# Kernel optimization log

Measured on AMD Instinct MI355X. Metric: run time of the kernel, lower is better.

The kernel has to match this reference:

```python
import jax, jax.numpy as jnp
import numpy as np
from jax import lax

N, L, D, F = 16, 512, 256, 256
KW = 3
EPS = 1e-5


def setup_inputs() -> dict:
    key = jax.random.key(0)
    ks = jax.random.split(key, 12)
    return {
        "x": jax.random.normal(ks[0], (N, L, D), jnp.float32),
        "conv1_w": jax.random.normal(ks[1], (F, D, KW), jnp.float32) * 0.05,
        "conv1_b": jnp.zeros((F,), jnp.float32),
        "ln1_g": jnp.ones((F,), jnp.float32),
        "ln1_b": jnp.zeros((F,), jnp.float32),
        "conv2_w": jax.random.normal(ks[2], (F, F, KW), jnp.float32) * 0.05,
        "conv2_b": jnp.zeros((F,), jnp.float32),
        "ln2_g": jnp.ones((F,), jnp.float32),
        "ln2_b": jnp.zeros((F,), jnp.float32),
        "lin_w": jax.random.normal(ks[3], (F, 1), jnp.float32) * 0.05,
        "lin_b": jnp.zeros((1,), jnp.float32),
        "target": jax.random.randint(ks[4], (N, L), 1, 8, jnp.int32),
        "mel_max_length": 4096,
    }


def _layernorm(h, g, b):
    m = jnp.mean(h, axis=-1, keepdims=True)
    v = jnp.var(h, axis=-1, keepdims=True)
    return (h - m) * lax.rsqrt(v + EPS) * g + b


def _conv1d(h, w, b):
    # h: [N, L, C_in]; w: [C_out, C_in, K]; 'same' padding=1 for K=3
    y = lax.conv_general_dilated(h.transpose(0, 2, 1), w, (1,), [(1, 1)],
                                 dimension_numbers=("NCH", "OIH", "NCH"))
    return (y + b[None, :, None]).transpose(0, 2, 1)


def _duration_predictor(x, c1w, c1b, g1, b1, c2w, c2b, g2, b2, lw, lb):
    h = jax.nn.relu(_layernorm(_conv1d(x, c1w, c1b), g1, b1))
    h = jax.nn.relu(_layernorm(_conv1d(h, c2w, c2b), g2, b2))
    return jax.nn.relu(h @ lw + lb)[..., 0]  # [N, L]


def _length_regulate(x, dur, T):
    # Equivalent to one-hot alignment @ x, done as a duration-indexed gather.
    cum = jnp.cumsum(dur, axis=-1)                       # [N, L]
    t = jnp.arange(T, dtype=cum.dtype)                   # [T]
    idx = jax.vmap(lambda c: jnp.searchsorted(c, t, side="right"))(cum)  # [N, T]
    valid = t[None, :] < cum[:, -1:]                     # [N, T]
    out = jnp.take_along_axis(x, jnp.clip(idx, 0, x.shape[1] - 1)[:, :, None], axis=1)
    return jnp.where(valid[..., None], out, jnp.zeros((), x.dtype))


def reference(x, conv1_w, conv1_b, ln1_g, ln1_b, conv2_w, conv2_b, ln2_g, ln2_b,
              lin_w, lin_b, target, mel_max_length):
    dpo = _duration_predictor(x, conv1_w, conv1_b, ln1_g, ln1_b,
                              conv2_w, conv2_b, ln2_g, ln2_b, lin_w, lin_b)
    out = _length_regulate(x, target, mel_max_length)    # [N, mel_max_length, D]
    return (out, dpo)
```

## Files before the change

### kernel.cpp

```cpp
#include <hip/hip_runtime.h>
#include <hip/hip_bf16.h>

using u16 = unsigned short;
typedef __bf16 bf16x8 __attribute__((ext_vector_type(8)));
typedef float f32x4 __attribute__((ext_vector_type(4)));

#define N_B   16
#define L_S   512
#define D_F   256
#define T_MEL 4096
#define M_TOT (N_B * L_S)
#define OUT_ELEMS ((size_t)N_B * T_MEL * D_F)
#define H1_ELEMS  ((size_t)M_TOT * D_F)
#define WP_ELEMS  (24 * 8192)
#define TBLK 128

__device__ __forceinline__ u16 f2bf(float f) {
  __hip_bfloat16 h = __float2bfloat16(f);
  return *(u16*)&h;
}

__device__ __forceinline__ bf16x8 pack8(float4 v0, float4 v1) {
  union { bf16x8 h; u16 u[8]; } r;
  r.u[0] = f2bf(v0.x); r.u[1] = f2bf(v0.y); r.u[2] = f2bf(v0.z); r.u[3] = f2bf(v0.w);
  r.u[4] = f2bf(v1.x); r.u[5] = f2bf(v1.y); r.u[6] = f2bf(v1.z); r.u[7] = f2bf(v1.w);
  return r.h;
}

__global__ __launch_bounds__(256)
void pack_kernel(const float* __restrict__ w1, const float* __restrict__ w2,
                 u16* __restrict__ wp1, u16* __restrict__ wp2) {
  int o   = (int)blockIdx.x * 256 + (int)threadIdx.x;
  int s   = o >> 13;
  int rem = o & 8191;
  int f   = rem >> 5;
  int ki  = rem & 31;
  int d   = ((s & 7) << 5) + ki;
  int tap = s >> 3;
  int src = f * 768 + d * 3 + tap;
  wp1[o] = f2bf(w1[src]);
  wp2[o] = f2bf(w2[src]);
}

template<int STAGE>
__device__ __forceinline__ void conv_body(
    const int blk, const int t,
    const float* __restrict__ Xf, const u16* __restrict__ Xh,
    const u16* __restrict__ Wp,
    const float* __restrict__ cb,  const float* __restrict__ lgm,
    const float* __restrict__ lbt, const float* __restrict__ lw,
    const float* __restrict__ lb,  u16* __restrict__ Hout,
    float* __restrict__ dpo,
    u16* As, u16* Bs, float* sBias, float* sG, float* sB, float* sLw,
    float (*redS)[4][16], float (*redQ)[4][16])
{
  if (t < 256) {
    sBias[t] = cb[t];
    sG[t]    = lgm[t];
    sB[t]    = lbt[t];
    if (STAGE == 2) sLw[t] = lw[t];
  }

  const int m0   = blk * 32;
  const int n    = m0 >> 9;
  const int l0   = m0 & 511;
  const int wave = t >> 6, lane = t & 63;
  const int cs   = wave & 3;
  const int rh   = wave >> 2;
  const int wc   = cs * 64;
  const int rh16 = rh * 16;
  const int p    = lane & 15, q = lane >> 4;

  f32x4 acc[4];
  #pragma unroll
  for (int i = 0; i < 4; i++) acc[i] = (f32x4){0.f, 0.f, 0.f, 0.f};

  auto LDW = [&](int s, uint4 &r0, uint4 &r1) {
    const u16* src = Wp + ((size_t)s << 13);
    r0 = *(const uint4*)(src + (t << 3));
    r1 = *(const uint4*)(src + ((t + 512) << 3));
  };
  auto WRB = [&](int buf, const uint4 &r0, const uint4 &r1) {
    *(uint4*)(Bs + (buf << 13) + (t << 3))         = r0;
    *(uint4*)(Bs + (buf << 13) + ((t + 512) << 3)) = r1;
  };
  auto MF = [&](int buf, int s) {
    const u16* bs = Bs + (buf << 13);
    const int tap = s >> 3, dbase = (s & 7) << 5;
    bf16x8 af = *(const bf16x8*)(As + (rh16 + p + tap) * 264 + dbase + (q << 3));
    #pragma unroll
    for (int ct = 0; ct < 4; ct++) {
      bf16x8 bfr = *(const bf16x8*)(bs + ((wc + ct * 16 + p) << 5) + (q << 3));
      acc[ct] = __builtin_amdgcn_mfma_f32_16x16x32_bf16(af, bfr, acc[ct], 0, 0, 0);
    }
  };

  uint4 e0, e1, o0, o1;
  LDW(0, e0, e1);
  LDW(1, o0, o1);

  for (int c = t; c < 1088; c += 512) {
    int row  = c >> 5;
    int col8 = c & 31;
    int l    = l0 + row - 1;
    uint4 val;
    if ((unsigned)l < 512u) {
      if (STAGE == 1) {
        const float* src = Xf + (((size_t)((n << 9) + l)) << 8) + (col8 << 3);
        float4 v0 = *(const float4*)src;
        float4 v1 = *(const float4*)(src + 4);
        bf16x8 pk = pack8(v0, v1);
        __builtin_memcpy(&val, &pk, 16);
      } else {
        val = *(const uint4*)(Xh + (((size_t)((n << 9) + l)) << 8) + (col8 << 3));
      }
    } else {
      val = make_uint4(0u, 0u, 0u, 0u);
    }
    *(uint4*)(As + row * 264 + (col8 << 3)) = val;
  }
  WRB(0, e0, e1);
  __syncthreads();

  for (int s2 = 0; s2 < 24; s2 += 2) {
    MF(0, s2);
    if (s2 + 2 < 24) LDW(s2 + 2, e0, e1);
    WRB(1, o0, o1);
    __syncthreads();
    MF(1, s2 + 1);
    if (s2 + 3 < 24) LDW(s2 + 3, o0, o1);
    if (s2 + 2 < 24) WRB(0, e0, e1);
    __syncthreads();
  }

  float s0[4] = {0,0,0,0}, s1[4] = {0,0,0,0};
  #pragma unroll
  for (int ct = 0; ct < 4; ct++) {
    float bias = sBias[wc + ct * 16 + p];
    #pragma unroll
    for (int j = 0; j < 4; j++) {
      float v = acc[ct][j] + bias;
      acc[ct][j] = v;
      s0[j] += v;
      s1[j] += v * v;
    }
  }
  #pragma unroll
  for (int m = 1; m <= 8; m <<= 1) {
    #pragma unroll
    for (int j = 0; j < 4; j++) {
      s0[j] += __shfl_xor(s0[j], m);
      s1[j] += __shfl_xor(s1[j], m);
    }
  }
  if (p == 0) {
    #pragma unroll
    for (int j = 0; j < 4; j++) {
      redS[rh][cs][q * 4 + j] = s0[j];
      redQ[rh][cs][q * 4 + j] = s1[j];
    }
  }
  __syncthreads();
  float mean[4], rstd[4];
  #pragma unroll
  for (int j = 0; j < 4; j++) {
    int r = q * 4 + j;
    float S = redS[rh][0][r] + redS[rh][1][r] + redS[rh][2][r] + redS[rh][3][r];
    float Q = redQ[rh][0][r] + redQ[rh][1][r] + redQ[rh][2][r] + redQ[rh][3][r];
    float mu  = S * (1.0f / 256.0f);
    float var = Q * (1.0f / 256.0f) - mu * mu;
    mean[j] = mu;
    rstd[j] = rsqrtf(var + 1e-5f);
  }

  if (STAGE == 1) {
    #pragma unroll
    for (int ct = 0; ct < 4; ct++) {
      int c = wc + ct * 16 + p;
      float gg = sG[c], bb = sB[c];
      #pragma unroll
      for (int j = 0; j < 4; j++) {
        float v = (acc[ct][j] - mean[j]) * rstd[j] * gg + bb;
        v = fmaxf(v, 0.0f);
        Hout[(size_t)(m0 + rh16 + q * 4 + j) * 256 + c] = f2bf(v);
      }
    }
  } else {
    float ls[4] = {0,0,0,0};
    #pragma unroll
    for (int ct = 0; ct < 4; ct++) {
      int c = wc + ct * 16 + p;
      float gg = sG[c], bb = sB[c], ww = sLw[c];
      #pragma unroll
      for (int j = 0; j < 4; j++) {
        float v = (acc[ct][j] - mean[j]) * rstd[j] * gg + bb;
        v = fmaxf(v, 0.0f);
        ls[j] += v * ww;
      }
    }
    #pragma unroll
    for (int m = 1; m <= 8; m <<= 1) {
      #pragma unroll
      for (int j = 0; j < 4; j++) ls[j] += __shfl_xor(ls[j], m);
    }
    __syncthreads();
    if (p == 0) {
      #pragma unroll
      for (int j = 0; j < 4; j++) redS[rh][cs][q * 4 + j] = ls[j];
    }
    __syncthreads();
    if (t < 32) {
      int r2 = t >> 4, ri = t & 15;
      float dv = fmaxf(redS[r2][0][ri] + redS[r2][1][ri] +
                       redS[r2][2][ri] + redS[r2][3][ri] + lb[0], 0.0f);
      dpo[m0 + t] = dv;
    }
  }
}

__device__ __forceinline__ void lr_body512(
    const int lrblk, const int t,
    const float* __restrict__ X, const int* __restrict__ tgt,
    float* __restrict__ out, int* sc, int* sidx)
{
  const int n  = lrblk >> 4;
  const int t0 = (lrblk & 15) * 256;

  sc[t] = tgt[n * L_S + t];
  __syncthreads();
  for (int off = 1; off < L_S; off <<= 1) {
    int v = (t >= off) ? sc[t - off] : 0;
    __syncthreads();
    sc[t] += v;
    __syncthreads();
  }
  const int total = sc[L_S - 1];
  if (t < 256) {
    int tt = t0 + t;
    int lo = 0, hi = L_S;
    while (lo < hi) {
      int mid = (lo + hi) >> 1;
      if (sc[mid] <= tt) lo = mid + 1; else hi = mid;
    }
    sidx[t] = (tt < total) ? lo : -1;
  }
  __syncthreads();

  #pragma unroll
  for (int i = 0; i < 32; i++) {
    int u   = t + i * 512;
    int dg  = u & 63;
    int tr  = u >> 6;
    int idx = sidx[tr];
    float4 v = make_float4(0.f, 0.f, 0.f, 0.f);
    if (idx >= 0)
      v = *(const float4*)(X + (((size_t)(n * L_S + idx)) << 8) + dg * 4);
    *(float4*)(out + (((size_t)(n * T_MEL + t0 + tr)) << 8) + dg * 4) = v;
  }
}

template<int STAGE>
__global__ __launch_bounds__(512)
void conv_ln_kernel(const float* __restrict__ Xf, const u16* __restrict__ Xh,
                    const u16* __restrict__ Wp,
                    const float* __restrict__ cb,  const float* __restrict__ lgm,
                    const float* __restrict__ lbt, const float* __restrict__ lw,
                    const float* __restrict__ lb,  u16* __restrict__ Hout,
                    float* __restrict__ dpo)
{
  __shared__ __align__(16) u16 As[34 * 264 + 8];
  __shared__ __align__(16) u16 Bs[2 * 8192];
  __shared__ float sBias[256], sG[256], sB[256], sLw[256];
  __shared__ float redS[2][4][16], redQ[2][4][16];
  conv_body<STAGE>((int)blockIdx.x, (int)threadIdx.x, Xf, Xh, Wp, cb, lgm, lbt,
                   lw, lb, Hout, dpo, As, Bs, sBias, sG, sB, sLw, redS, redQ);
}

__global__ __launch_bounds__(512)
void conv1_lr_kernel(const float* __restrict__ x, const u16* __restrict__ Wp,
                     const float* __restrict__ cb,  const float* __restrict__ lgm,
                     const float* __restrict__ lbt, u16* __restrict__ Hout,
                     const int* __restrict__ tgt, float* __restrict__ out)
{
  __shared__ __align__(16) u16 As[34 * 264 + 8];
  __shared__ __align__(16) u16 Bs[2 * 8192];
  __shared__ float sBias[256], sG[256], sB[256], sLw[256];
  __shared__ float redS[2][4][16], redQ[2][4][16];
  __shared__ int  sc[512];
  __shared__ int  sidx[256];

  const int blk = (int)blockIdx.x, t = (int)threadIdx.x;
  if (blk < 256) {
    conv_body<1>(blk, t, x, nullptr, Wp, cb, lgm, lbt, nullptr, nullptr,
                 Hout, nullptr, As, Bs, sBias, sG, sB, sLw, redS, redQ);
  } else {
    lr_body512(blk - 256, t, x, tgt, out, sc, sidx);
  }
}

__global__ __launch_bounds__(256)
void lr_kernel(const float* __restrict__ X, const int* __restrict__ tgt,
               float* __restrict__ out) {
  __shared__ int c[L_S];
  __shared__ int sidx[TBLK];
  const int t  = threadIdx.x;
  const int n  = blockIdx.x >> 5;
  const int t0 = (blockIdx.x & 31) * TBLK;

  c[t]       = tgt[n * L_S + t];
  c[t + 256] = tgt[n * L_S + t + 256];
  __syncthreads();
  for (int off = 1; off < L_S; off <<= 1) {
    int v0 = (t >= off) ? c[t - off] : 0;
    int i1 = t + 256;
    int v1 = (i1 >= off) ? c[i1 - off] : 0;
    __syncthreads();
    c[t]  += v0;
    c[i1] += v1;
    __syncthreads();
  }
  const int total = c[L_S - 1];
  if (t < TBLK) {
    int tt = t0 + t;
    int lo = 0, hi = L_S;
    while (lo < hi) {
      int mid = (lo + hi) >> 1;
      if (c[mid] <= tt) lo = mid + 1; else hi = mid;
    }
    sidx[t] = (tt < total) ? lo : -1;
  }
  __syncthreads();

  #pragma unroll
  for (int i = 0; i < 32; i++) {
    int u   = t + i * 256;
    int dg  = u & 63;
    int tr  = u >> 6;
    int idx = sidx[tr];
    float4 v = make_float4(0.f, 0.f, 0.f, 0.f);
    if (idx >= 0)
      v = *(const float4*)(X + (((size_t)(n * L_S + idx)) << 8) + dg * 4);
    *(float4*)(out + (((size_t)(n * T_MEL + t0 + tr)) << 8) + dg * 4) = v;
  }
}

extern "C" void kernel_launch(void* const* d_in, const int* in_sizes, int n_in,
                              void* d_out, int out_size, void* d_ws, size_t ws_size,
                              hipStream_t stream) {
  (void)in_sizes; (void)n_in; (void)out_size;

  const float* x   = (const float*)d_in[0];
  const float* w1  = (const float*)d_in[1];
  const float* b1  = (const float*)d_in[2];
  const float* g1  = (const float*)d_in[3];
  const float* be1 = (const float*)d_in[4];
  const float* w2  = (const float*)d_in[5];
  const float* b2  = (const float*)d_in[6];
  const float* g2  = (const float*)d_in[7];
  const float* be2 = (const float*)d_in[8];
  const float* lw  = (const float*)d_in[9];
  const float* lb  = (const float*)d_in[10];
  const int*   tgt = (const int*)d_in[11];

  float* out = (float*)d_out;
  float* dpo = out + OUT_ELEMS;

  const size_t need = (H1_ELEMS + 2 * (size_t)WP_ELEMS) * sizeof(u16);

  if (d_ws != nullptr && ws_size >= need) {
    u16* h1  = (u16*)d_ws;
    u16* wp1 = h1 + H1_ELEMS;
    u16* wp2 = wp1 + WP_ELEMS;
    pack_kernel<<<768, 256, 0, stream>>>(w1, w2, wp1, wp2);
    conv1_lr_kernel<<<512, 512, 0, stream>>>(x, wp1, b1, g1, be1, h1, tgt, out);
    conv_ln_kernel<2><<<M_TOT / 32, 512, 0, stream>>>(
        nullptr, h1, wp2, b2, g2, be2, lw, lb, nullptr, dpo);
  } else {
    u16* h1  = (u16*)d_out;
    u16* wp1 = h1 + H1_ELEMS;
    u16* wp2 = wp1 + WP_ELEMS;
    pack_kernel<<<768, 256, 0, stream>>>(w1, w2, wp1, wp2);
    conv_ln_kernel<1><<<M_TOT / 32, 512, 0, stream>>>(
        x, nullptr, wp1, b1, g1, be1, nullptr, nullptr, h1, nullptr);
    conv_ln_kernel<2><<<M_TOT / 32, 512, 0, stream>>>(
        nullptr, h1, wp2, b2, g2, be2, lw, lb, nullptr, dpo);
    lr_kernel<<<N_B * (T_MEL / TBLK), 256, 0, stream>>>(x, tgt, out);
  }
}
```

Baseline: 121.0 us.

## Fuse both conv+layernorm stages and length regulation into one kernel

Merges the conv1 and conv2 stages into a single kernel: each block recomputes conv1 over a 66-row halo window (32 output rows plus a one-row halo on each side, rounded up for MFMA tiles) and keeps the intermediate H tile in shared memory. This removes the global round-trip of the bf16 intermediate and one kernel launch. In exchange it does about twice the conv1 MFMA work per block and uses more shared memory, which may lower occupancy. The length-regulation blocks still share the same launch.

```diff
diff --git a/kernel.cpp b/kernel.cpp
--- a/kernel.cpp
+++ b/kernel.cpp
@@ -40,6 +40,325 @@
   int src = f * 768 + d * 3 + tap;
   wp1[o] = f2bf(w1[src]);
   wp2[o] = f2bf(w2[src]);
+}
+
+__device__ __forceinline__ void lr_body512(
+    const int lrblk, const int t,
+    const float* __restrict__ X, const int* __restrict__ tgt,
+    float* __restrict__ out, int* sc, int* sidx)
+{
+  const int n  = lrblk >> 4;
+  const int t0 = (lrblk & 15) * 256;
+
+  sc[t] = tgt[n * L_S + t];
+  __syncthreads();
+  for (int off = 1; off < L_S; off <<= 1) {
+    int v = (t >= off) ? sc[t - off] : 0;
+    __syncthreads();
+    sc[t] += v;
+    __syncthreads();
+  }
+  const int total = sc[L_S - 1];
+  if (t < 256) {
+    int tt = t0 + t;
+    int lo = 0, hi = L_S;
+    while (lo < hi) {
+      int mid = (lo + hi) >> 1;
+      if (sc[mid] <= tt) lo = mid + 1; else hi = mid;
+    }
+    sidx[t] = (tt < total) ? lo : -1;
+  }
+  __syncthreads();
+
+  #pragma unroll
+  for (int i = 0; i < 32; i++) {
+    int u   = t + i * 512;
+    int dg  = u & 63;
+    int tr  = u >> 6;
+    int idx = sidx[tr];
+    float4 v = make_float4(0.f, 0.f, 0.f, 0.f);
+    if (idx >= 0)
+      v = *(const float4*)(X + (((size_t)(n * L_S + idx)) << 8) + dg * 4);
+    *(float4*)(out + (((size_t)(n * T_MEL + t0 + tr)) << 8) + dg * 4) = v;
+  }
+}
+
+__global__ __launch_bounds__(512)
+void fused_conv_lr_kernel(
+    const float* __restrict__ x,
+    const u16* __restrict__ wp1, const u16* __restrict__ wp2,
+    const float* __restrict__ b1, const float* __restrict__ g1,
+    const float* __restrict__ e1p,
+    const float* __restrict__ b2, const float* __restrict__ g2,
+    const float* __restrict__ e2p,
+    const float* __restrict__ lw, const float* __restrict__ lb,
+    const int* __restrict__ tgt, float* __restrict__ out,
+    float* __restrict__ dpo)
+{
+  __shared__ __align__(16) u16 As66[66 * 264];
+  __shared__ __align__(16) u16 Hs[34 * 264];
+  __shared__ __align__(16) u16 Bs[2 * 8192];
+  __shared__ float sB1[256], sG1[256], sE1[256];
+  __shared__ float sB2[256], sG2[256], sE2[256], sLw[256];
+  __shared__ float redS[4][4][16], redQ[4][4][16];
+  __shared__ int  sc[512];
+  __shared__ int  sidx[256];
+
+  const int blk = (int)blockIdx.x, t = (int)threadIdx.x;
+  if (blk >= 256) {
+    lr_body512(blk - 256, t, x, tgt, out, sc, sidx);
+    return;
+  }
+
+  if (t < 256) {
+    sB1[t] = b1[t];  sG1[t] = g1[t];  sE1[t] = e1p[t];
+    sB2[t] = b2[t];  sG2[t] = g2[t];  sE2[t] = e2p[t];
+    sLw[t] = lw[t];
+  }
+
+  const int m0   = blk * 32;
+  const int n    = m0 >> 9;
+  const int l0   = m0 & 511;
+  const int wave = t >> 6, lane = t & 63;
+  const int cs   = wave & 3;
+  const int rha  = wave >> 2;
+  const int wc   = cs * 64;
+  const int p    = lane & 15, q = lane >> 4;
+
+  auto LDW = [&](const u16* Wp, int s, uint4 &r0, uint4 &r1) {
+    const u16* src = Wp + ((size_t)s << 13);
+    r0 = *(const uint4*)(src + (t << 3));
+    r1 = *(const uint4*)(src + ((t + 512) << 3));
+  };
+  auto WRB = [&](int buf, const uint4 &r0, const uint4 &r1) {
+    *(uint4*)(Bs + (buf << 13) + (t << 3))         = r0;
+    *(uint4*)(Bs + (buf << 13) + ((t + 512) << 3)) = r1;
+  };
+
+  f32x4 acc1[2][4];
+  #pragma unroll
+  for (int gi = 0; gi < 2; gi++)
+    #pragma unroll
+    for (int i = 0; i < 4; i++) acc1[gi][i] = (f32x4){0.f, 0.f, 0.f, 0.f};
+
+  auto MF1 = [&](int buf, int s) {
+    const u16* bs = Bs + (buf << 13);
+    const int tap = s >> 3, dbase = (s & 7) << 5;
+    bf16x8 af0 = *(const bf16x8*)(As66 + ((rha << 4)        + p + tap) * 264 + dbase + (q << 3));
+    bf16x8 af1 = *(const bf16x8*)(As66 + (((rha + 2) << 4)  + p + tap) * 264 + dbase + (q << 3));
+    #pragma unroll
+    for (int ct = 0; ct < 4; ct++) {
+      bf16x8 bfr = *(const bf16x8*)(bs + ((wc + ct * 16 + p) << 5) + (q << 3));
+      acc1[0][ct] = __builtin_amdgcn_mfma_f32_16x16x32_bf16(af0, bfr, acc1[0][ct], 0, 0, 0);
+      acc1[1][ct] = __builtin_amdgcn_mfma_f32_16x16x32_bf16(af1, bfr, acc1[1][ct], 0, 0, 0);
+    }
+  };
+
+  uint4 e0, e1, o0, o1;
+  LDW(wp1, 0, e0, e1);
+  LDW(wp1, 1, o0, o1);
+
+  for (int c = t; c < 66 * 32; c += 512) {
+    int row  = c >> 5;
+    int col8 = c & 31;
+    int l    = l0 - 17 + row;
+    uint4 val = make_uint4(0u, 0u, 0u, 0u);
+    if ((unsigned)l < 512u) {
+      const float* src = x + (((size_t)((n << 9) + l)) << 8) + (col8 << 3);
+      float4 v0 = *(const float4*)src;
+      float4 v1 = *(const float4*)(src + 4);
+      bf16x8 pk = pack8(v0, v1);
+      __builtin_memcpy(&val, &pk, 16);
+    }
+    *(uint4*)(As66 + row * 264 + (col8 << 3)) = val;
+  }
+  WRB(0, e0, e1);
+  __syncthreads();
+
+  for (int s2 = 0; s2 < 24; s2 += 2) {
+    MF1(0, s2);
+    if (s2 + 2 < 24) LDW(wp1, s2 + 2, e0, e1);
+    WRB(1, o0, o1);
+    __syncthreads();
+    MF1(1, s2 + 1);
+    if (s2 + 3 < 24) LDW(wp1, s2 + 3, o0, o1);
+    if (s2 + 2 < 24) WRB(0, e0, e1);
+    __syncthreads();
+  }
+
+  {
+    float s0[2][4] = {{0,0,0,0},{0,0,0,0}}, s1[2][4] = {{0,0,0,0},{0,0,0,0}};
+    #pragma unroll
+    for (int gi = 0; gi < 2; gi++)
+      #pragma unroll
+      for (int ct = 0; ct < 4; ct++) {
+        float bias = sB1[wc + ct * 16 + p];
+        #pragma unroll
+        for (int j = 0; j < 4; j++) {
+          float v = acc1[gi][ct][j] + bias;
+          acc1[gi][ct][j] = v;
+          s0[gi][j] += v;
+          s1[gi][j] += v * v;
+        }
+      }
+    #pragma unroll
+    for (int m = 1; m <= 8; m <<= 1)
+      #pragma unroll
+      for (int gi = 0; gi < 2; gi++)
+        #pragma unroll
+        for (int j = 0; j < 4; j++) {
+          s0[gi][j] += __shfl_xor(s0[gi][j], m);
+          s1[gi][j] += __shfl_xor(s1[gi][j], m);
+        }
+    if (p == 0) {
+      #pragma unroll
+      for (int gi = 0; gi < 2; gi++) {
+        int g = rha + gi * 2;
+        #pragma unroll
+        for (int j = 0; j < 4; j++) {
+          redS[g][cs][q * 4 + j] = s0[gi][j];
+          redQ[g][cs][q * 4 + j] = s1[gi][j];
+        }
+      }
+    }
+    __syncthreads();
+    float mean[2][4], rstd[2][4];
+    #pragma unroll
+    for (int gi = 0; gi < 2; gi++) {
+      int g = rha + gi * 2;
+      #pragma unroll
+      for (int j = 0; j < 4; j++) {
+        int r = q * 4 + j;
+        float S = redS[g][0][r] + redS[g][1][r] + redS[g][2][r] + redS[g][3][r];
+        float Q = redQ[g][0][r] + redQ[g][1][r] + redQ[g][2][r] + redQ[g][3][r];
+        float mu  = S * (1.0f / 256.0f);
+        float var = Q * (1.0f / 256.0f) - mu * mu;
+        mean[gi][j] = mu;
+        rstd[gi][j] = rsqrtf(var + 1e-5f);
+      }
+    }
+    #pragma unroll
+    for (int gi = 0; gi < 2; gi++) {
+      int g = rha + gi * 2;
+      #pragma unroll
+      for (int ct = 0; ct < 4; ct++) {
+        int c = wc + ct * 16 + p;
+        float gg = sG1[c], bb = sE1[c];
+        #pragma unroll
+        for (int j = 0; j < 4; j++) {
+          float v = (acc1[gi][ct][j] - mean[gi][j]) * rstd[gi][j] * gg + bb;
+          v = fmaxf(v, 0.0f);
+          int hidx = (g << 4) - 15 + q * 4 + j;
+          if ((unsigned)hidx < 34u)
+            Hs[hidx * 264 + c] = f2bf(v);
+        }
+      }
+    }
+    __syncthreads();
+    if (l0 == 0   && t < 132) ((unsigned*)Hs)[t] = 0u;
+    if (l0 == 480 && t < 132) ((unsigned*)Hs)[33 * 132 + t] = 0u;
+    __syncthreads();
+  }
+
+  f32x4 acc2[4];
+  #pragma unroll
+  for (int i = 0; i < 4; i++) acc2[i] = (f32x4){0.f, 0.f, 0.f, 0.f};
+
+  auto MF2 = [&](int buf, int s) {
+    const u16* bs = Bs + (buf << 13);
+    const int tap = s >> 3, dbase = (s & 7) << 5;
+    bf16x8 af = *(const bf16x8*)(Hs + ((rha << 4) + p + tap) * 264 + dbase + (q << 3));
+    #pragma unroll
+    for (int ct = 0; ct < 4; ct++) {
+      bf16x8 bfr = *(const bf16x8*)(bs + ((wc + ct * 16 + p) << 5) + (q << 3));
+      acc2[ct] = __builtin_amdgcn_mfma_f32_16x16x32_bf16(af, bfr, acc2[ct], 0, 0, 0);
+    }
+  };
+
+  LDW(wp2, 0, e0, e1);
+  LDW(wp2, 1, o0, o1);
+  WRB(0, e0, e1);
+  __syncthreads();
+
+  for (int s2 = 0; s2 < 24; s2 += 2) {
+    MF2(0, s2);
+    if (s2 + 2 < 24) LDW(wp2, s2 + 2, e0, e1);
+    WRB(1, o0, o1);
+    __syncthreads();
+    MF2(1, s2 + 1);
+    if (s2 + 3 < 24) LDW(wp2, s2 + 3, o0, o1);
+    if (s2 + 2 < 24) WRB(0, e0, e1);
+    __syncthreads();
+  }
+
+  {
+    float s0[4] = {0,0,0,0}, s1[4] = {0,0,0,0};
+    #pragma unroll
+    for (int ct = 0; ct < 4; ct++) {
+      float bias = sB2[wc + ct * 16 + p];
+      #pragma unroll
+      for (int j = 0; j < 4; j++) {
+        float v = acc2[ct][j] + bias;
+        acc2[ct][j] = v;
+        s0[j] += v;
+        s1[j] += v * v;
+      }
+    }
+    #pragma unroll
+    for (int m = 1; m <= 8; m <<= 1)
+      #pragma unroll
+      for (int j = 0; j < 4; j++) {
+        s0[j] += __shfl_xor(s0[j], m);
+        s1[j] += __shfl_xor(s1[j], m);
+      }
+    if (p == 0) {
+      #pragma unroll
+      for (int j = 0; j < 4; j++) {
+        redS[rha][cs][q * 4 + j] = s0[j];
+        redQ[rha][cs][q * 4 + j] = s1[j];
+      }
+    }
+    __syncthreads();
+    float mean[4], rstd[4];
+    #pragma unroll
+    for (int j = 0; j < 4; j++) {
+      int r = q * 4 + j;
+      float S = redS[rha][0][r] + redS[rha][1][r] + redS[rha][2][r] + redS[rha][3][r];
+      float Q = redQ[rha][0][r] + redQ[rha][1][r] + redQ[rha][2][r] + redQ[rha][3][r];
+      float mu  = S * (1.0f / 256.0f);
+      float var = Q * (1.0f / 256.0f) - mu * mu;
+      mean[j] = mu;
+      rstd[j] = rsqrtf(var + 1e-5f);
+    }
+    float ls[4] = {0,0,0,0};
+    #pragma unroll
+    for (int ct = 0; ct < 4; ct++) {
+      int c = wc + ct * 16 + p;
+      float gg = sG2[c], bb = sE2[c], ww = sLw[c];
+      #pragma unroll
+      for (int j = 0; j < 4; j++) {
+        float v = (acc2[ct][j] - mean[j]) * rstd[j] * gg + bb;
+        v = fmaxf(v, 0.0f);
+        ls[j] += v * ww;
+      }
+    }
+    #pragma unroll
+    for (int m = 1; m <= 8; m <<= 1)
+      #pragma unroll
+      for (int j = 0; j < 4; j++) ls[j] += __shfl_xor(ls[j], m);
+    __syncthreads();
+    if (p == 0) {
+      #pragma unroll
+      for (int j = 0; j < 4; j++) redS[rha][cs][q * 4 + j] = ls[j];
+    }
+    __syncthreads();
+    if (t < 32) {
+      int r2 = t >> 4, ri = t & 15;
+      float dv = fmaxf(redS[r2][0][ri] + redS[r2][1][ri] +
+                       redS[r2][2][ri] + redS[r2][3][ri] + lb[0], 0.0f);
+      dpo[m0 + t] = dv;
+    }
+  }
 }
 
 template<int STAGE>
@@ -218,47 +537,6 @@
   }
 }
 
-__device__ __forceinline__ void lr_body512(
-    const int lrblk, const int t,
-    const float* __restrict__ X, const int* __restrict__ tgt,
-    float* __restrict__ out, int* sc, int* sidx)
-{
-  const int n  = lrblk >> 4;
-  const int t0 = (lrblk & 15) * 256;
-
-  sc[t] = tgt[n * L_S + t];
-  __syncthreads();
-  for (int off = 1; off < L_S; off <<= 1) {
-    int v = (t >= off) ? sc[t - off] : 0;
-    __syncthreads();
-    sc[t] += v;
-    __syncthreads();
-  }
-  const int total = sc[L_S - 1];
-  if (t < 256) {
-    int tt = t0 + t;
-    int lo = 0, hi = L_S;
-    while (lo < hi) {
-      int mid = (lo + hi) >> 1;
-      if (sc[mid] <= tt) lo = mid + 1; else hi = mid;
-    }
-    sidx[t] = (tt < total) ? lo : -1;
-  }
-  __syncthreads();
-
-  #pragma unroll
-  for (int i = 0; i < 32; i++) {
-    int u   = t + i * 512;
-    int dg  = u & 63;
-    int tr  = u >> 6;
-    int idx = sidx[tr];
-    float4 v = make_float4(0.f, 0.f, 0.f, 0.f);
-    if (idx >= 0)
-      v = *(const float4*)(X + (((size_t)(n * L_S + idx)) << 8) + dg * 4);
-    *(float4*)(out + (((size_t)(n * T_MEL + t0 + tr)) << 8) + dg * 4) = v;
-  }
-}
-
 template<int STAGE>
 __global__ __launch_bounds__(512)
 void conv_ln_kernel(const float* __restrict__ Xf, const u16* __restrict__ Xh,
@@ -276,28 +554,6 @@
                    lw, lb, Hout, dpo, As, Bs, sBias, sG, sB, sLw, redS, redQ);
 }
 
-__global__ __launch_bounds__(512)
-void conv1_lr_kernel(const float* __restrict__ x, const u16* __restrict__ Wp,
-                     const float* __restrict__ cb,  const float* __restrict__ lgm,
-                     const float* __restrict__ lbt, u16* __restrict__ Hout,
-                     const int* __restrict__ tgt, float* __restrict__ out)
-{
-  __shared__ __align__(16) u16 As[34 * 264 + 8];
-  __shared__ __align__(16) u16 Bs[2 * 8192];
-  __shared__ float sBias[256], sG[256], sB[256], sLw[256];
-  __shared__ float redS[2][4][16], redQ[2][4][16];
-  __shared__ int  sc[512];
-  __shared__ int  sidx[256];
-
-  const int blk = (int)blockIdx.x, t = (int)threadIdx.x;
-  if (blk < 256) {
-    conv_body<1>(blk, t, x, nullptr, Wp, cb, lgm, lbt, nullptr, nullptr,
-                 Hout, nullptr, As, Bs, sBias, sG, sB, sLw, redS, redQ);
-  } else {
-    lr_body512(blk - 256, t, x, tgt, out, sc, sidx);
-  }
-}
-
 __global__ __launch_bounds__(256)
 void lr_kernel(const float* __restrict__ X, const int* __restrict__ tgt,
                float* __restrict__ out) {
@@ -365,16 +621,14 @@
   float* out = (float*)d_out;
   float* dpo = out + OUT_ELEMS;
 
-  const size_t need = (H1_ELEMS + 2 * (size_t)WP_ELEMS) * sizeof(u16);
-
-  if (d_ws != nullptr && ws_size >= need) {
-    u16* h1  = (u16*)d_ws;
-    u16* wp1 = h1 + H1_ELEMS;
+  const size_t need_ws = 2 * (size_t)WP_ELEMS * sizeof(u16);
+
+  if (d_ws != nullptr && ws_size >= need_ws) {
+    u16* wp1 = (u16*)d_ws;
     u16* wp2 = wp1 + WP_ELEMS;
     pack_kernel<<<768, 256, 0, stream>>>(w1, w2, wp1, wp2);
-    conv1_lr_kernel<<<512, 512, 0, stream>>>(x, wp1, b1, g1, be1, h1, tgt, out);
-    conv_ln_kernel<2><<<M_TOT / 32, 512, 0, stream>>>(
-        nullptr, h1, wp2, b2, g2, be2, lw, lb, nullptr, dpo);
+    fused_conv_lr_kernel<<<512, 512, 0, stream>>>(
+        x, wp1, wp2, b1, g1, be1, b2, g2, be2, lw, lb, tgt, out, dpo);
   } else {
     u16* h1  = (u16*)d_out;
     u16* wp1 = h1 + H1_ELEMS;
```

After: 132.3 us. 1.09x slower.
